# Kernel tuning notes

Measured on AMD Instinct MI355X. Metric: run time of the kernel, lower is better.

Reference implementation:

```python
import jax, jax.numpy as jnp
import numpy as np

CUTOFF = 5.0
ENV_EXP = 5          # envelope_exponent
NUM_RADIAL = 6
EMB = 128
NUM_ATOM_TYPES = 95
N_NODES = 50000
N_EDGES = 800000


def envelope(x):
    # p = exponent + 1
    p = ENV_EXP + 1
    a = -(p + 1) * (p + 2) / 2.0
    b = p * (p + 2) * 1.0
    c = -p * (p + 1) / 2.0
    x_p_0 = x ** (p - 1)
    x_p_1 = x_p_0 * x
    x_p_2 = x_p_1 * x
    return 1.0 / x + a * x_p_0 + b * x_p_1 + c * x_p_2


def setup_inputs() -> dict:
    key = jax.random.key(0)
    ks = jax.random.split(key, 10)
    Z = jax.random.randint(ks[0], (N_NODES,), 0, NUM_ATOM_TYPES)
    src = jax.random.randint(ks[1], (N_EDGES,), 0, N_NODES)
    dst = jax.random.randint(ks[2], (N_EDGES,), 0, N_NODES)
    rbf = jax.random.normal(ks[3], (N_EDGES, NUM_RADIAL), dtype=jnp.float32)
    # distances in (0, cutoff]; keep away from 0 to avoid 1/x blowup
    d = jax.random.uniform(ks[4], (N_EDGES,), dtype=jnp.float32,
                           minval=0.05, maxval=1.0) * CUTOFF
    sqrt3 = float(np.sqrt(3.0))
    emb_table = jax.random.uniform(ks[5], (NUM_ATOM_TYPES, EMB),
                                   dtype=jnp.float32, minval=-sqrt3, maxval=sqrt3)
    W_rbf = jax.random.normal(ks[6], (EMB, NUM_RADIAL), dtype=jnp.float32) * (1.0 / np.sqrt(NUM_RADIAL))
    b_rbf = jnp.zeros((EMB,), dtype=jnp.float32)
    W_dense = jax.random.normal(ks[7], (EMB, 3 * EMB), dtype=jnp.float32) * (1.0 / np.sqrt(3 * EMB))
    b_dense = jnp.zeros((EMB,), dtype=jnp.float32)
    return {"Z": Z, "src": src, "dst": dst, "rbf": rbf, "d": d,
            "emb_table": emb_table, "W_rbf": W_rbf, "b_rbf": b_rbf,
            "W_dense": W_dense, "b_dense": b_dense}


def reference(Z, src, dst, rbf, d, emb_table, W_rbf, b_rbf, W_dense, b_dense):
    act = jax.nn.silu
    # node embeddings: g.ndata['h'] = embedding(Z)
    h = emb_table[Z]                                   # [N, EMB]
    # edge_init
    rbf_proj = act(rbf @ W_rbf.T + b_rbf)              # [E, EMB]
    m = jnp.concatenate([h[src], h[dst], rbf_proj], axis=-1)  # [E, 3*EMB]
    m = act(m @ W_dense.T + b_dense)                   # [E, EMB]
    d_scaled = d / CUTOFF                              # [E]
    # bessel funcs: sin(n*pi*x)/x, n = 1..NUM_RADIAL (stacked along dim=1)
    freqs = jnp.pi * jnp.arange(1, NUM_RADIAL + 1, dtype=d.dtype)  # [R]
    rbf_env = jnp.sin(d_scaled[:, None] * freqs) / d_scaled[:, None]  # [E, R]
    d_cutoff = envelope(d_scaled)                      # [E]
    rbf_env = d_cutoff[:, None] * rbf_env              # [E, R]
    return h, m, rbf_env
```

## Files before the change

### kernel.cpp

```cpp
#include <hip/hip_runtime.h>
#include <hip/hip_bf16.h>
#include <math.h>

#define CUTOFFV 5.0f
#define NRAD 6
#define EMB 128
#define NTYPES 95
#define PI_F 3.14159265358979323846f

typedef short short8 __attribute__((ext_vector_type(8)));
typedef float f32x4 __attribute__((ext_vector_type(4)));
typedef float f32x2 __attribute__((ext_vector_type(2)));

__device__ __forceinline__ unsigned short f2bf(float f) {
    union { float f; unsigned int u; } v; v.f = f;
    unsigned int u = v.u;
    unsigned int r = (u + 0x7FFFu + ((u >> 16) & 1u)) >> 16;
    return (unsigned short)r;
}

__device__ __forceinline__ short bf16s(float f) {
    union { __hip_bfloat16 h; short s; } u;
    u.h = __float2bfloat16(f);
    return u.s;
}

__device__ __forceinline__ float fast_rcp(float x) {
    float y;
    asm("v_rcp_f32 %0, %1" : "=v"(y) : "v"(x));
    return y;
}

__device__ __forceinline__ float silu_f(float x) {
    return x * fast_rcp(1.0f + __expf(-x));
}

__device__ __forceinline__ void lds_barrier() {
    __builtin_amdgcn_sched_barrier(0);
    asm volatile("s_waitcnt lgkmcnt(0)\n\ts_barrier" ::: "memory");
    __builtin_amdgcn_sched_barrier(0);
}

__global__ void prep_kernel(const float* __restrict__ emb,
                            const float* __restrict__ Wd,
                            const float* __restrict__ bd,
                            const float* __restrict__ Wr,
                            const float* __restrict__ brbf,
                            float* __restrict__ P1, float* __restrict__ P2,
                            unsigned short* __restrict__ W3b,
                            float* __restrict__ Wrp) {
    int b = blockIdx.x, tid = threadIdx.x;
    if (b < 2 * NTYPES) {
        int t = b / NTYPES, z = b % NTYPES;
        __shared__ float emb_s[EMB];
        emb_s[tid] = emb[z * EMB + tid];
        __syncthreads();
        float acc = (t == 0) ? bd[tid] : 0.0f;
        const float* wrow = Wd + (size_t)tid * 384 + t * EMB;
        #pragma unroll 8
        for (int j = 0; j < EMB; ++j) acc += emb_s[j] * wrow[j];
        (t == 0 ? P1 : P2)[z * EMB + tid] = acc;
    } else if (b < 2 * NTYPES + 8) {
        int g = (b - 2 * NTYPES) * 128 + tid;
        for (int i = g; i < EMB * EMB; i += 8 * 128) {
            int n = i >> 7, k = i & 127;
            W3b[i] = f2bf(Wd[(size_t)n * 384 + 256 + k]);
        }
    } else {
        if (tid < EMB) {
            int k = tid;
            #pragma unroll
            for (int j = 0; j < 6; ++j) Wrp[k * 8 + j] = Wr[k * 6 + j];
            Wrp[k * 8 + 6] = brbf[k];
            Wrp[k * 8 + 7] = 0.0f;
        }
    }
}

__global__ void h_kernel(const int* __restrict__ Z, const float* __restrict__ emb,
                         float* __restrict__ out_h, int N) {
    int idx = blockIdx.x * 256 + threadIdx.x;
    int total = N * (EMB / 4);
    if (idx >= total) return;
    int v = idx >> 5, c = idx & 31;
    int z = Z[v];
    const f32x4* e4 = (const f32x4*)emb;
    f32x4* o4 = (f32x4*)out_h;
    o4[idx] = e4[z * 32 + c];
}

__global__ void env_kernel(const float* __restrict__ dvec,
                           float* __restrict__ out_env, int E) {
    int e = blockIdx.x * 256 + threadIdx.x;
    if (e >= E) return;
    float x = dvec[e] * (1.0f / CUTOFFV);
    float inv = fast_rcp(x);
    float x2 = x * x;
    float x5 = x2 * x2 * x;
    float env = inv + x5 * (-28.0f + x * (48.0f - 21.0f * x));
    float s1, c1;
    __sincosf(PI_F * x, &s1, &c1);
    float twoc = 2.0f * c1;
    float f = env * inv;
    float s2 = twoc * s1;
    float s3 = twoc * s2 - s1;
    float s4 = twoc * s3 - s2;
    float s5 = twoc * s4 - s3;
    float s6 = twoc * s5 - s4;
    float* o = out_env + (size_t)e * 6;
    __builtin_nontemporal_store((f32x2){f * s1, f * s2}, (f32x2*)o);
    __builtin_nontemporal_store((f32x2){f * s3, f * s4}, (f32x2*)(o + 2));
    __builtin_nontemporal_store((f32x2){f * s5, f * s6}, (f32x2*)(o + 4));
}

__global__ void __launch_bounds__(256, 7)
edge_kernel(const int* __restrict__ Z, const int* __restrict__ src,
            const int* __restrict__ dst, const float* __restrict__ rbf,
            const float* __restrict__ P1, const float* __restrict__ P2,
            const unsigned short* __restrict__ W3b,
            const float* __restrict__ Wrp,
            float* __restrict__ out_m,
            int E, int ntiles) {
    __shared__ unsigned char A_lds[64 * 256];
    __shared__ int zs_s[64], zd_s[64];

    const int tid = threadIdx.x;
    const int lane = tid & 63;
    const int w = tid >> 6;
    const int lr = lane & 15;
    const int lg = lane >> 4;
    const int wu = __builtin_amdgcn_readfirstlane(w);

    short8 wfrag[2][4];
    #pragma unroll
    for (int nt = 0; nt < 2; ++nt) {
        int n = w * 32 + nt * 16 + lr;
        #pragma unroll
        for (int ks = 0; ks < 4; ++ks)
            wfrag[nt][ks] = *(const short8*)(W3b + n * EMB + ks * 32 + lg * 8);
    }

    f32x2 ra, rb, rc;
    int iv = 0;
    {
        const int e0p = blockIdx.x * 64;
        int ecl = e0p + lane; if (ecl >= E) ecl = E - 1;
        const f32x2* r2 = (const f32x2*)(rbf + (size_t)ecl * 6);
        ra = r2[0]; rb = r2[1]; rc = r2[2];
        if (tid < 128) {
            int ec = e0p + (tid & 63); if (ec >= E) ec = E - 1;
            iv = (tid < 64) ? src[ec] : dst[ec];
        }
    }

    for (int t = blockIdx.x; t < ntiles; t += gridDim.x) {
        const int tn = t + gridDim.x;

        f32x2 nra, nrb, nrc;
        int niv = 0;
        if (tn < ntiles) {
            const int e0n = tn * 64;
            int ecl = e0n + lane; if (ecl >= E) ecl = E - 1;
            const f32x2* r2 = (const f32x2*)(rbf + (size_t)ecl * 6);
            nra = r2[0]; nrb = r2[1]; nrc = r2[2];
            if (tid < 128) {
                int ec = e0n + (tid & 63); if (ec >= E) ec = E - 1;
                niv = (tid < 64) ? src[ec] : dst[ec];
            }
        }

        int zreg = 0;
        if (tid < 128) zreg = Z[iv];

        #pragma unroll
        for (int c = 0; c < 4; ++c) {
            const float* wp0 = Wrp + (size_t)(wu * 32 + c * 8) * 8;
            short8 pk;
            #pragma unroll
            for (int j = 0; j < 8; ++j) {
                const float* wp = wp0 + j * 8;
                float pre = wp[6] + ra.x * wp[0] + ra.y * wp[1] +
                            rb.x * wp[2] + rb.y * wp[3] +
                            rc.x * wp[4] + rc.y * wp[5];
                pk[j] = bf16s(silu_f(pre));
            }
            int k0 = wu * 32 + c * 8;
            int off = (lane * 256 + k0 * 2) ^ ((lane & 7) << 4);
            *(short8*)(A_lds + off) = pk;
        }
        if (tid < 64) zs_s[tid] = zreg;
        else if (tid < 128) zd_s[tid - 64] = zreg;

        lds_barrier();

        const int e0c = t * 64;
        #pragma unroll
        for (int et = 0; et < 4; ++et) {
            const int e_row = et * 16 + lr;
            short8 bfrag[4];
            #pragma unroll
            for (int ks = 0; ks < 4; ++ks) {
                int off = (e_row * 256 + (ks * 32 + lg * 8) * 2) ^ ((e_row & 7) << 4);
                bfrag[ks] = *(const short8*)(A_lds + off);
            }
            f32x4 acc[2];
            acc[0] = (f32x4){0.f, 0.f, 0.f, 0.f};
            acc[1] = (f32x4){0.f, 0.f, 0.f, 0.f};
            #pragma unroll
            for (int ks = 0; ks < 4; ++ks)
                #pragma unroll
                for (int nt = 0; nt < 2; ++nt)
                    acc[nt] = __builtin_amdgcn_mfma_f32_16x16x32_bf16(
                        wfrag[nt][ks], bfrag[ks], acc[nt], 0, 0, 0);

            const int el = e_row;
            const int e = e0c + el;
            const int zs = zs_s[el], zd = zd_s[el];
            #pragma unroll
            for (int nt = 0; nt < 2; ++nt) {
                int n4 = w * 32 + nt * 16 + lg * 4;
                const f32x4 p1 = *(const f32x4*)(P1 + zs * EMB + n4);
                const f32x4 p2 = *(const f32x4*)(P2 + zd * EMB + n4);
                f32x4 o;
                o.x = silu_f(acc[nt][0] + p1.x + p2.x);
                o.y = silu_f(acc[nt][1] + p1.y + p2.y);
                o.z = silu_f(acc[nt][2] + p1.z + p2.z);
                o.w = silu_f(acc[nt][3] + p1.w + p2.w);
                if (e < E)
                    __builtin_nontemporal_store(
                        o, (f32x4*)(out_m + (size_t)e * EMB + n4));
            }
        }

        lds_barrier();

        ra = nra; rb = nrb; rc = nrc; iv = niv;
    }
}

extern "C" void kernel_launch(void* const* d_in, const int* in_sizes, int n_in,
                              void* d_out, int out_size, void* d_ws, size_t ws_size,
                              hipStream_t stream) {
    const int* Z = (const int*)d_in[0];
    const int* src = (const int*)d_in[1];
    const int* dst = (const int*)d_in[2];
    const float* rbf = (const float*)d_in[3];
    const float* dvec = (const float*)d_in[4];
    const float* emb = (const float*)d_in[5];
    const float* Wr = (const float*)d_in[6];
    const float* brbf = (const float*)d_in[7];
    const float* Wd = (const float*)d_in[8];
    const float* bd = (const float*)d_in[9];

    const int N = in_sizes[0];
    const int E = in_sizes[1];

    float* out_h = (float*)d_out;
    float* out_m = out_h + (size_t)N * EMB;
    float* out_env = out_m + (size_t)E * EMB;

    float* P1 = (float*)d_ws;
    float* P2 = P1 + NTYPES * EMB;
    unsigned short* W3b = (unsigned short*)(P2 + NTYPES * EMB);
    float* Wrp = (float*)(W3b + EMB * EMB);

    prep_kernel<<<2 * NTYPES + 9, 128, 0, stream>>>(emb, Wd, bd, Wr, brbf,
                                                    P1, P2, W3b, Wrp);

    int hblocks = (N * (EMB / 4) + 255) / 256;
    h_kernel<<<hblocks, 256, 0, stream>>>(Z, emb, out_h, N);

    int eblocks = (E + 255) / 256;
    env_kernel<<<eblocks, 256, 0, stream>>>(dvec, out_env, E);

    int ntiles = (E + 63) / 64;
    int grid = ntiles < 1792 ? ntiles : 1792;
    edge_kernel<<<grid, 256, 0, stream>>>(Z, src, dst, rbf,
                                          P1, P2, W3b, Wrp,
                                          out_m, E, ntiles);
}
```

Measured before the change: 189.8 us.

## Double-buffer LDS tiles in edge kernel and use regular stores

Restructures the persistent edge kernel into a software pipeline. Each iteration consumes the previous tile from one LDS buffer, running the MFMA, epilogue and stores, while producing the next tile's rbf projection into the other buffer, so only one barrier per iteration is needed. Nontemporal stores are replaced with plain stores in both the env and edge kernels. The launch bound drops from 7 to 4 blocks per CU and the grid from 1792 to 1024 blocks, which lowers occupancy in exchange for doubled LDS use and more overlap within each block.

```diff
diff --git a/kernel.cpp b/kernel.cpp
--- a/kernel.cpp
+++ b/kernel.cpp
@@ -108,12 +108,12 @@
     float s5 = twoc * s4 - s3;
     float s6 = twoc * s5 - s4;
     float* o = out_env + (size_t)e * 6;
-    __builtin_nontemporal_store((f32x2){f * s1, f * s2}, (f32x2*)o);
-    __builtin_nontemporal_store((f32x2){f * s3, f * s4}, (f32x2*)(o + 2));
-    __builtin_nontemporal_store((f32x2){f * s5, f * s6}, (f32x2*)(o + 4));
-}
-
-__global__ void __launch_bounds__(256, 7)
+    *(f32x2*)o       = (f32x2){f * s1, f * s2};
+    *(f32x2*)(o + 2) = (f32x2){f * s3, f * s4};
+    *(f32x2*)(o + 4) = (f32x2){f * s5, f * s6};
+}
+
+__global__ void __launch_bounds__(256, 4)
 edge_kernel(const int* __restrict__ Z, const int* __restrict__ src,
             const int* __restrict__ dst, const float* __restrict__ rbf,
             const float* __restrict__ P1, const float* __restrict__ P2,
@@ -121,8 +121,8 @@
             const float* __restrict__ Wrp,
             float* __restrict__ out_m,
             int E, int ntiles) {
-    __shared__ unsigned char A_lds[64 * 256];
-    __shared__ int zs_s[64], zd_s[64];
+    __shared__ unsigned char A_lds[2][64 * 256];
+    __shared__ int zs_s[2][64], zd_s[2][64];
 
     const int tid = threadIdx.x;
     const int lane = tid & 63;
@@ -140,101 +140,94 @@
             wfrag[nt][ks] = *(const short8*)(W3b + n * EMB + ks * 32 + lg * 8);
     }
 
-    f32x2 ra, rb, rc;
-    int iv = 0;
-    {
-        const int e0p = blockIdx.x * 64;
-        int ecl = e0p + lane; if (ecl >= E) ecl = E - 1;
-        const f32x2* r2 = (const f32x2*)(rbf + (size_t)ecl * 6);
-        ra = r2[0]; rb = r2[1]; rc = r2[2];
-        if (tid < 128) {
-            int ec = e0p + (tid & 63); if (ec >= E) ec = E - 1;
-            iv = (tid < 64) ? src[ec] : dst[ec];
-        }
-    }
-
-    for (int t = blockIdx.x; t < ntiles; t += gridDim.x) {
-        const int tn = t + gridDim.x;
-
-        f32x2 nra, nrb, nrc;
-        int niv = 0;
-        if (tn < ntiles) {
-            const int e0n = tn * 64;
-            int ecl = e0n + lane; if (ecl >= E) ecl = E - 1;
+    for (int i = 0; ; ++i) {
+        const int tp = blockIdx.x + i * gridDim.x;
+        const int tc = tp - gridDim.x;
+        const bool do_p = (tp < ntiles);
+        const bool do_c = (i > 0) && (tc < ntiles);
+        if (!do_p && !do_c) break;
+        const int pi = i & 1, ci = pi ^ 1;
+
+        f32x2 ra = {0.f, 0.f}, rb = {0.f, 0.f}, rc = {0.f, 0.f};
+        int iv = 0;
+        if (do_p) {
+            const int e0p = tp * 64;
+            int ecl = e0p + lane; if (ecl >= E) ecl = E - 1;
             const f32x2* r2 = (const f32x2*)(rbf + (size_t)ecl * 6);
-            nra = r2[0]; nrb = r2[1]; nrc = r2[2];
+            ra = r2[0]; rb = r2[1]; rc = r2[2];
             if (tid < 128) {
-                int ec = e0n + (tid & 63); if (ec >= E) ec = E - 1;
-                niv = (tid < 64) ? src[ec] : dst[ec];
+                int ec = e0p + (tid & 63); if (ec >= E) ec = E - 1;
+                iv = (tid < 64) ? src[ec] : dst[ec];
             }
         }
 
-        int zreg = 0;
-        if (tid < 128) zreg = Z[iv];
-
-        #pragma unroll
-        for (int c = 0; c < 4; ++c) {
-            const float* wp0 = Wrp + (size_t)(wu * 32 + c * 8) * 8;
-            short8 pk;
+        if (do_c) {
+            const int e0c = tc * 64;
+            const unsigned char* Ab = A_lds[ci];
             #pragma unroll
-            for (int j = 0; j < 8; ++j) {
-                const float* wp = wp0 + j * 8;
-                float pre = wp[6] + ra.x * wp[0] + ra.y * wp[1] +
-                            rb.x * wp[2] + rb.y * wp[3] +
-                            rc.x * wp[4] + rc.y * wp[5];
-                pk[j] = bf16s(silu_f(pre));
+            for (int et = 0; et < 4; ++et) {
+                const int e_row = et * 16 + lr;
+                short8 bfrag[4];
+                #pragma unroll
+                for (int ks = 0; ks < 4; ++ks) {
+                    int off = (e_row * 256 + (ks * 32 + lg * 8) * 2) ^ ((e_row & 7) << 4);
+                    bfrag[ks] = *(const short8*)(Ab + off);
+                }
+                f32x4 acc[2];
+                acc[0] = (f32x4){0.f, 0.f, 0.f, 0.f};
+                acc[1] = (f32x4){0.f, 0.f, 0.f, 0.f};
+                #pragma unroll
+                for (int ks = 0; ks < 4; ++ks)
+                    #pragma unroll
+                    for (int nt = 0; nt < 2; ++nt)
+                        acc[nt] = __builtin_amdgcn_mfma_f32_16x16x32_bf16(
+                            wfrag[nt][ks], bfrag[ks], acc[nt], 0, 0, 0);
+
+                const int el = e_row;
+                const int e = e0c + el;
+                const int zs = zs_s[ci][el], zd = zd_s[ci][el];
+                #pragma unroll
+                for (int nt = 0; nt < 2; ++nt) {
+                    int n4 = w * 32 + nt * 16 + lg * 4;
+                    const f32x4 p1 = *(const f32x4*)(P1 + zs * EMB + n4);
+                    const f32x4 p2 = *(const f32x4*)(P2 + zd * EMB + n4);
+                    f32x4 o;
+                    o.x = silu_f(acc[nt][0] + p1.x + p2.x);
+                    o.y = silu_f(acc[nt][1] + p1.y + p2.y);
+                    o.z = silu_f(acc[nt][2] + p1.z + p2.z);
+                    o.w = silu_f(acc[nt][3] + p1.w + p2.w);
+                    if (e < E)
+                        *(f32x4*)(out_m + (size_t)e * EMB + n4) = o;
+                }
             }
-            int k0 = wu * 32 + c * 8;
-            int off = (lane * 256 + k0 * 2) ^ ((lane & 7) << 4);
-            *(short8*)(A_lds + off) = pk;
-        }
-        if (tid < 64) zs_s[tid] = zreg;
-        else if (tid < 128) zd_s[tid - 64] = zreg;
+        }
+
+        if (do_p) {
+            int zreg = 0;
+            if (tid < 128) zreg = Z[iv];
+
+            #pragma unroll
+            for (int c = 0; c < 4; ++c) {
+                const float* wp0 = Wrp + (size_t)(wu * 32 + c * 8) * 8;
+                short8 pk;
+                #pragma unroll
+                for (int j = 0; j < 8; ++j) {
+                    const float* wp = wp0 + j * 8;
+                    float pre = wp[6] + ra.x * wp[0] + ra.y * wp[1] +
+                                rb.x * wp[2] + rb.y * wp[3] +
+                                rc.x * wp[4] + rc.y * wp[5];
+                    pk[j] = bf16s(silu_f(pre));
+                }
+                int k0 = wu * 32 + c * 8;
+                int off = (lane * 256 + k0 * 2) ^ ((lane & 7) << 4);
+                *(short8*)(A_lds[pi] + off) = pk;
+            }
+
+            if (tid < 64) zs_s[pi][tid] = zreg;
+            else if (tid < 128) zd_s[pi][tid - 64] = zreg;
+        }
 
         lds_barrier();
-
-        const int e0c = t * 64;
-        #pragma unroll
-        for (int et = 0; et < 4; ++et) {
-            const int e_row = et * 16 + lr;
-            short8 bfrag[4];
-            #pragma unroll
-            for (int ks = 0; ks < 4; ++ks) {
-                int off = (e_row * 256 + (ks * 32 + lg * 8) * 2) ^ ((e_row & 7) << 4);
-                bfrag[ks] = *(const short8*)(A_lds + off);
-            }
-            f32x4 acc[2];
-            acc[0] = (f32x4){0.f, 0.f, 0.f, 0.f};
-            acc[1] = (f32x4){0.f, 0.f, 0.f, 0.f};
-            #pragma unroll
-            for (int ks = 0; ks < 4; ++ks)
-                #pragma unroll
-                for (int nt = 0; nt < 2; ++nt)
-                    acc[nt] = __builtin_amdgcn_mfma_f32_16x16x32_bf16(
-                        wfrag[nt][ks], bfrag[ks], acc[nt], 0, 0, 0);
-
-            const int el = e_row;
-            const int e = e0c + el;
-            const int zs = zs_s[el], zd = zd_s[el];
-            #pragma unroll
-            for (int nt = 0; nt < 2; ++nt) {
-                int n4 = w * 32 + nt * 16 + lg * 4;
-                const f32x4 p1 = *(const f32x4*)(P1 + zs * EMB + n4);
-                const f32x4 p2 = *(const f32x4*)(P2 + zd * EMB + n4);
-                f32x4 o;
-                o.x = silu_f(acc[nt][0] + p1.x + p2.x);
-                o.y = silu_f(acc[nt][1] + p1.y + p2.y);
-                o.z = silu_f(acc[nt][2] + p1.z + p2.z);
-                o.w = silu_f(acc[nt][3] + p1.w + p2.w);
-                if (e < E)
-                    __builtin_nontemporal_store(
-                        o, (f32x4*)(out_m + (size_t)e * EMB + n4));
-            }
-        }
-
-        lds_barrier();
-
-        ra = nra; rb = nrb; rc = nrc; iv = niv;
     }
 }
 
@@ -274,7 +267,7 @@
     env_kernel<<<eblocks, 256, 0, stream>>>(dvec, out_env, E);
 
     int ntiles = (E + 63) / 64;
-    int grid = ntiles < 1792 ? ntiles : 1792;
+    int grid = ntiles < 1024 ? ntiles : 1024;
     edge_kernel<<<grid, 256, 0, stream>>>(Z, src, dst, rbf,
                                           P1, P2, W3b, Wrp,
                                           out_m, E, ntiles);
```

Result: slower. 209.8 us (+10.5%).
